# Kernel tuning notes

Hardware: AMD Instinct MI355X
Metric: run time of the kernel (lower is better)

Reference implementation:

```python
import jax, jax.numpy as jnp
import numpy as np

EMBED_DIM = 768
NUM_HEADS = 12
HEAD_DIM = EMBED_DIM // NUM_HEADS
MEMORY_SIZE = 64
B, T = 8, 1024


def setup_inputs() -> dict:
    key = jax.random.key(0)
    ks = jax.random.split(key, 8)
    s = 0.02
    return {
        "x": jax.random.normal(ks[0], (B, T, EMBED_DIM), dtype=jnp.float32),
        "w_qkv": jax.random.normal(ks[1], (EMBED_DIM, 3 * EMBED_DIM), dtype=jnp.float32) * s,
        "b_qkv": jax.random.normal(ks[2], (3 * EMBED_DIM,), dtype=jnp.float32) * s,
        "w_out": jax.random.normal(ks[3], (EMBED_DIM, EMBED_DIM), dtype=jnp.float32) * s,
        "b_out": jax.random.normal(ks[4], (EMBED_DIM,), dtype=jnp.float32) * s,
        "w_mem": jax.random.normal(ks[5], (EMBED_DIM, EMBED_DIM), dtype=jnp.float32) * s,
        "b_mem": jax.random.normal(ks[6], (EMBED_DIM,), dtype=jnp.float32) * s,
        "memory": jax.random.normal(ks[7], (1, MEMORY_SIZE, EMBED_DIM), dtype=jnp.float32),
    }


def reference(x, w_qkv, b_qkv, w_out, b_out, w_mem, b_mem, memory):
    Bx, Tx, C = x.shape
    H, D = NUM_HEADS, HEAD_DIM
    scale = 1.0 / np.sqrt(D).astype(np.float32)

    # qkv projection -> (3, B, H, T, D)
    qkv = (x @ w_qkv + b_qkv).reshape(Bx, Tx, 3, H, D)
    qkv = jnp.transpose(qkv, (2, 0, 3, 1, 4))
    q, k, v = qkv[0], qkv[1], qkv[2]

    # full (non-causal) local attention over T
    scores = jnp.einsum("bhqd,bhkd->bhqk", q, k) * scale  # (B,H,T,T)
    local_out = jnp.einsum("bhqk,bhkd->bhqd", jax.nn.softmax(scores, axis=-1), v)

    # memory attention: projected memory serves as both K and V
    mem = memory @ w_mem + b_mem                      # (1, M, C)
    mem = jnp.broadcast_to(mem, (Bx, MEMORY_SIZE, C))
    mem_kv = jnp.transpose(mem.reshape(Bx, MEMORY_SIZE, H, D), (0, 2, 1, 3))  # (B,H,M,D)
    mem_scores = jnp.einsum("bhqd,bhmd->bhqm", q, mem_kv) * scale
    mem_out = jnp.einsum("bhqm,bhmd->bhqd", jax.nn.softmax(mem_scores, axis=-1), mem_kv)

    out = (local_out + mem_out).transpose(0, 2, 1, 3).reshape(Bx, Tx, C)
    return out @ w_out + b_out
```

## Files before the change

### kernel.cpp

```cpp
#include <hip/hip_runtime.h>

#define EMBED 768
#define NH 12
#define HD 64
#define MEMN 64
#define BB 8
#define TT 1024
#define ROWS 8192
#define QKV_N 2304
#define QSZ 6291456

typedef short bf16x8_t __attribute__((ext_vector_type(8)));
typedef float f32x4_t __attribute__((ext_vector_type(4)));

__device__ __forceinline__ unsigned short f2b(float f){
    union { float f; unsigned int i; } v; v.f = f;
    unsigned int x = v.i;
    unsigned int r = x + 0x7fffu + ((x >> 16) & 1u);
    return (unsigned short)(r >> 16);
}
__device__ __forceinline__ unsigned short f2b_ru(float f){
    union { float f; unsigned int i; } v; v.f = f;
    return (unsigned short)((v.i + 0x8000u) >> 16);
}

__device__ __forceinline__ void gl16(const unsigned short* g, unsigned short* l){
    __builtin_amdgcn_global_load_lds(
        (const __attribute__((address_space(1))) void*)g,
        (__attribute__((address_space(3))) void*)l,
        16, 0, 0);
}

#define PREP_CVT   3072
#define PREP_TQKV  4800
#define PREP_TOUT  5376
#define PREP_TOTAL 5388

__global__ __launch_bounds__(256) void prep_kernel(
    const float* __restrict__ x,
    const float* __restrict__ w_qkv,
    const float* __restrict__ w_out,
    const float* __restrict__ memory,
    const float* __restrict__ w_mem,
    const float* __restrict__ b_mem,
    unsigned short* __restrict__ xb,
    unsigned short* __restrict__ wqkvT,
    unsigned short* __restrict__ woutT,
    unsigned short* __restrict__ mem_k,
    unsigned short* __restrict__ mem_v)
{
    __shared__ unsigned short pool[5120];
    const int bid = blockIdx.x;
    const int t = threadIdx.x;

    if (bid < PREP_CVT) {
        int i = bid * 2048 + t * 8;
        float4 f0 = *(const float4*)&x[i];
        float4 f1 = *(const float4*)&x[i + 4];
        union { bf16x8_t v; unsigned short s[8]; } u;
        u.s[0] = f2b(f0.x); u.s[1] = f2b(f0.y); u.s[2] = f2b(f0.z); u.s[3] = f2b(f0.w);
        u.s[4] = f2b(f1.x); u.s[5] = f2b(f1.y); u.s[6] = f2b(f1.z); u.s[7] = f2b(f1.w);
        *(bf16x8_t*)&xb[i] = u.v;
    } else if (bid < PREP_TOUT) {
        const float* in; unsigned short* out; int R, C, loc;
        if (bid < PREP_TQKV) { in = w_qkv; out = wqkvT; R = EMBED; C = QKV_N; loc = bid - PREP_CVT; }
        else                 { in = w_out; out = woutT; R = EMBED; C = EMBED; loc = bid - PREP_TQKV; }
        int nbc = C / 32;
        int bc = (loc % nbc) * 32, br = (loc / nbc) * 32;
        unsigned short (*tile)[33] = (unsigned short(*)[33])pool;
        int lr = t >> 5, lc = t & 31;
        for (int i = 0; i < 4; i++) {
            int r = lr + i * 8;
            tile[r][lc] = f2b(in[(size_t)(br + r) * C + bc + lc]);
        }
        __syncthreads();
        for (int i = 0; i < 4; i++) {
            int r = lr + i * 8;
            out[(size_t)(bc + r) * R + br + lc] = tile[lc][r];
        }
    } else {
        unsigned short (*As)[40] = (unsigned short(*)[40])pool;
        unsigned short (*Bs)[40] = (unsigned short(*)[40])(pool + 2560);
        int wave = t >> 6, lane = t & 63;
        int ln = lane & 15, lq = lane >> 4;
        int bn = (bid - PREP_TOUT) * 64;
        const int K = EMBED, N = EMBED;

        f32x4_t acc[4];
        for (int i = 0; i < 4; i++) acc[i] = (f32x4_t)(0.f);
        int sm = t >> 2, sk = (t & 3) * 8;
        int bk = t >> 3, bn8 = (t & 7) * 8;

        for (int k0 = 0; k0 < K; k0 += 32) {
            __syncthreads();
            {
                float4 f0 = *(const float4*)&memory[(size_t)sm * K + k0 + sk];
                float4 f1 = *(const float4*)&memory[(size_t)sm * K + k0 + sk + 4];
                unsigned short* ap = &As[sm][sk];
                ap[0] = f2b(f0.x); ap[1] = f2b(f0.y); ap[2] = f2b(f0.z); ap[3] = f2b(f0.w);
                ap[4] = f2b(f1.x); ap[5] = f2b(f1.y); ap[6] = f2b(f1.z); ap[7] = f2b(f1.w);
            }
            {
                float4 g0 = *(const float4*)&w_mem[(size_t)(k0 + bk) * N + bn + bn8];
                float4 g1 = *(const float4*)&w_mem[(size_t)(k0 + bk) * N + bn + bn8 + 4];
                Bs[bn8 + 0][bk] = f2b(g0.x); Bs[bn8 + 1][bk] = f2b(g0.y);
                Bs[bn8 + 2][bk] = f2b(g0.z); Bs[bn8 + 3][bk] = f2b(g0.w);
                Bs[bn8 + 4][bk] = f2b(g1.x); Bs[bn8 + 5][bk] = f2b(g1.y);
                Bs[bn8 + 6][bk] = f2b(g1.z); Bs[bn8 + 7][bk] = f2b(g1.w);
            }
            __syncthreads();
            bf16x8_t a = *(bf16x8_t*)&As[wave * 16 + ln][lq * 8];
            for (int nt = 0; nt < 4; nt++) {
                bf16x8_t bf = *(bf16x8_t*)&Bs[nt * 16 + ln][lq * 8];
                acc[nt] = __builtin_amdgcn_mfma_f32_16x16x32_bf16(a, bf, acc[nt], 0, 0, 0);
            }
        }
        for (int nt = 0; nt < 4; nt++) {
            int c = bn + nt * 16 + ln;
            float bv = b_mem[c];
            for (int r = 0; r < 4; r++) {
                int row = wave * 16 + lq * 4 + r;
                int h = c >> 6, d = c & 63;
                unsigned short o = f2b(acc[nt][r] + bv);
                mem_k[((h * 64 + row) << 6) + d] = o;
                mem_v[((h * 64 + d) << 6) + row] = o;
            }
        }
    }
}

__global__ __launch_bounds__(256) void vtrans_kernel(
    const unsigned short* __restrict__ in, unsigned short* __restrict__ out)
{
    __shared__ unsigned short tile[64][72];
    int t0 = blockIdx.x * 64;
    int bh = blockIdx.y;
    const unsigned short* ip = in + ((size_t)bh * TT + t0) * 64;
    unsigned short* op = out + ((size_t)bh * 64) * TT + t0;
    int t = threadIdx.x;
    for (int i = 0; i < 2; i++) {
        int idx = i * 256 + t;
        int r = idx >> 3, c8 = (idx & 7) * 8;
        *(bf16x8_t*)&tile[r][c8] = *(const bf16x8_t*)&ip[(size_t)r * 64 + c8];
    }
    __syncthreads();
    for (int i = 0; i < 2; i++) {
        int idx = i * 256 + t;
        int d = idx >> 3, tc8 = (idx & 7) * 8;
        union { bf16x8_t v; unsigned short s[8]; } u;
        for (int j = 0; j < 8; j++) u.s[j] = tile[tc8 + j][d];
        *(bf16x8_t*)&op[(size_t)d * TT + tc8] = u.v;
    }
}

__global__ __launch_bounds__(512) void gemm512(
    const unsigned short* __restrict__ A,
    const unsigned short* __restrict__ BT,
    const float* __restrict__ bias,
    unsigned short* __restrict__ dq,
    unsigned short* __restrict__ dkv,
    int M, int N, int K)
{
    __shared__ unsigned short As[2][16384];
    __shared__ unsigned short Bs[2][8192];
    const int t = threadIdx.x;
    const int wave = t >> 6, lane = t & 63;
    const int ln = lane & 15, lq = lane >> 4;
    const int wm = (wave >> 1) * 64, wn = (wave & 1) * 64;

    int bid0 = blockIdx.y * gridDim.x + blockIdx.x;
    int bid = (bid0 & 7) * 72 + (bid0 >> 3);
    int by = bid / 18, bx = bid - by * 18;
    const int bm = by * 256, bn = bx * 128;

    f32x4_t acc[4][4];
    for (int i = 0; i < 4; i++)
        for (int j = 0; j < 4; j++) acc[i][j] = (f32x4_t)(0.f);

    const int rl8 = lane >> 3;
    const int swz = ((lane & 7) ^ rl8) * 8;
    const unsigned short* Ap = A + (size_t)(bm + wave * 32 + rl8) * K + swz;
    const unsigned short* Bp = BT + (size_t)(bn + wave * 16 + rl8) * K + swz;

    const int e0 = (lq ^ (ln & 7)) * 8;
    const int e1 = e0 ^ 32;

    auto compute = [&](const unsigned short* Ac, const unsigned short* Bc) {
        bf16x8_t af0[4], af1[4], bf0[4], bf1[4];
#pragma unroll
        for (int mt = 0; mt < 4; mt++) {
            af0[mt] = *(const bf16x8_t*)&Ac[(wm + mt * 16 + ln) * 64 + e0];
            af1[mt] = *(const bf16x8_t*)&Ac[(wm + mt * 16 + ln) * 64 + e1];
        }
#pragma unroll
        for (int nt = 0; nt < 4; nt++) {
            bf0[nt] = *(const bf16x8_t*)&Bc[(wn + nt * 16 + ln) * 64 + e0];
            bf1[nt] = *(const bf16x8_t*)&Bc[(wn + nt * 16 + ln) * 64 + e1];
        }
        __builtin_amdgcn_s_setprio(1);
#pragma unroll
        for (int mt = 0; mt < 4; mt++)
#pragma unroll
            for (int nt = 0; nt < 4; nt++)
                acc[mt][nt] = __builtin_amdgcn_mfma_f32_16x16x32_bf16(
                    af0[mt], bf0[nt], acc[mt][nt], 0, 0, 0);
#pragma unroll
        for (int mt = 0; mt < 4; mt++)
#pragma unroll
            for (int nt = 0; nt < 4; nt++)
                acc[mt][nt] = __builtin_amdgcn_mfma_f32_16x16x32_bf16(
                    af1[mt], bf1[nt], acc[mt][nt], 0, 0, 0);
        __builtin_amdgcn_s_setprio(0);
    };

    for (int i = 0; i < 4; i++)
        gl16(Ap + (size_t)(i * 8) * K, &As[0][wave * 2048 + i * 512]);
    for (int i = 0; i < 2; i++)
        gl16(Bp + (size_t)(i * 8) * K, &Bs[0][wave * 1024 + i * 512]);
    __syncthreads();

    int cur = 0;
    for (int k0 = 0; k0 < K - 64; k0 += 64) {
        const int nb = cur ^ 1;
        for (int i = 0; i < 4; i++)
            gl16(Ap + (size_t)(i * 8) * K + k0 + 64, &As[nb][wave * 2048 + i * 512]);
        for (int i = 0; i < 2; i++)
            gl16(Bp + (size_t)(i * 8) * K + k0 + 64, &Bs[nb][wave * 1024 + i * 512]);
        compute(As[cur], Bs[cur]);
        __syncthreads();
        cur = nb;
    }
    compute(As[cur], Bs[cur]);

    const float QSCALE = 0.125f * 1.44269504088896340736f;
    const int s = bn / 768;
    for (int nt = 0; nt < 4; nt++) {
        int c = bn + wn + nt * 16 + ln;
        int rem = c - s * 768;
        int h = rem >> 6, d = rem & 63;
        float bv = bias[c];
        for (int mt = 0; mt < 4; mt++) {
            for (int r = 0; r < 4; r++) {
                int row = bm + wm + mt * 16 + lq * 4 + r;
                float val = acc[mt][nt][r] + bv;
                if (s == 0) {
                    dq[(size_t)row * 768 + rem] = f2b(val * QSCALE);
                } else {
                    int bb = row >> 10, tt = row & 1023;
                    dkv[(size_t)(s - 1) * QSZ +
                        (((size_t)(bb * 12 + h) * 1024 + tt) << 6) + d] = f2b(val);
                }
            }
        }
    }
}

__global__ __launch_bounds__(256) void gemm_bt(
    const unsigned short* __restrict__ A,
    const unsigned short* __restrict__ BT,
    const float* __restrict__ bias,
    float* __restrict__ df,
    int M, int N, int K)
{
    __shared__ unsigned short As[2][8192];
    __shared__ unsigned short Bs[2][8192];
    const int t = threadIdx.x;
    const int wave = t >> 6, lane = t & 63;
    const int ln = lane & 15, lq = lane >> 4;
    const int wm = (wave >> 1) * 64, wn = (wave & 1) * 64;
    const int bm = blockIdx.y * 128, bn = blockIdx.x * 128;

    f32x4_t acc[4][4];
    for (int i = 0; i < 4; i++)
        for (int j = 0; j < 4; j++) acc[i][j] = (f32x4_t)(0.f);

    const int rl8 = lane >> 3;
    const int swz = ((lane & 7) ^ rl8) * 8;
    const unsigned short* Ap = A + (size_t)(bm + wave * 32 + rl8) * K + swz;
    const unsigned short* Bp = BT + (size_t)(bn + wave * 32 + rl8) * K + swz;

    const int e0 = (lq ^ (ln & 7)) * 8;
    const int e1 = e0 ^ 32;

    auto compute = [&](const unsigned short* Ac, const unsigned short* Bc) {
        bf16x8_t af0[4], af1[4], bf0[4], bf1[4];
#pragma unroll
        for (int mt = 0; mt < 4; mt++) {
            af0[mt] = *(const bf16x8_t*)&Ac[(wm + mt * 16 + ln) * 64 + e0];
            af1[mt] = *(const bf16x8_t*)&Ac[(wm + mt * 16 + ln) * 64 + e1];
        }
#pragma unroll
        for (int nt = 0; nt < 4; nt++) {
            bf0[nt] = *(const bf16x8_t*)&Bc[(wn + nt * 16 + ln) * 64 + e0];
            bf1[nt] = *(const bf16x8_t*)&Bc[(wn + nt * 16 + ln) * 64 + e1];
        }
        __builtin_amdgcn_s_setprio(1);
#pragma unroll
        for (int mt = 0; mt < 4; mt++)
#pragma unroll
            for (int nt = 0; nt < 4; nt++)
                acc[mt][nt] = __builtin_amdgcn_mfma_f32_16x16x32_bf16(
                    af0[mt], bf0[nt], acc[mt][nt], 0, 0, 0);
#pragma unroll
        for (int mt = 0; mt < 4; mt++)
#pragma unroll
            for (int nt = 0; nt < 4; nt++)
                acc[mt][nt] = __builtin_amdgcn_mfma_f32_16x16x32_bf16(
                    af1[mt], bf1[nt], acc[mt][nt], 0, 0, 0);
        __builtin_amdgcn_s_setprio(0);
    };

    for (int i = 0; i < 4; i++) {
        gl16(Ap + (size_t)(i * 8) * K, &As[0][wave * 2048 + i * 512]);
        gl16(Bp + (size_t)(i * 8) * K, &Bs[0][wave * 2048 + i * 512]);
    }
    __syncthreads();

    int cur = 0;
    for (int k0 = 0; k0 < K - 64; k0 += 64) {
        const int nb = cur ^ 1;
        for (int i = 0; i < 4; i++) {
            gl16(Ap + (size_t)(i * 8) * K + k0 + 64, &As[nb][wave * 2048 + i * 512]);
            gl16(Bp + (size_t)(i * 8) * K + k0 + 64, &Bs[nb][wave * 2048 + i * 512]);
        }
        compute(As[cur], Bs[cur]);
        __syncthreads();
        cur = nb;
    }
    compute(As[cur], Bs[cur]);

    for (int nt = 0; nt < 4; nt++) {
        int c = bn + wn + nt * 16 + ln;
        float bv = bias[c];
        for (int mt = 0; mt < 4; mt++)
            for (int r = 0; r < 4; r++) {
                int row = bm + wm + mt * 16 + lq * 4 + r;
                df[(size_t)row * N + c] = acc[mt][nt][r] + bv;
            }
    }
}

__global__ __launch_bounds__(512) void attn_kernel(
    unsigned short* __restrict__ qio,
    const unsigned short* __restrict__ k_ws,
    const unsigned short* __restrict__ vT_ws,
    const unsigned short* __restrict__ mem_k,
    const unsigned short* __restrict__ mem_v)
{
    __shared__ unsigned short Qs[8192];
    __shared__ unsigned short Ks[8192];
    __shared__ unsigned short Vs[8192];
    unsigned short* Ps = Qs;

    const int t = threadIdx.x;
    const int wave = t >> 6, lane = t & 63;
    const int ln = lane & 15, lq = lane >> 4;
    const int rl = lane >> 3;
    const int cl = ((lane & 7) ^ rl) * 8;

    int bid = blockIdx.x;
    int xcd = bid & 7, rest = bid >> 3;
    int bh = xcd * 12 + (rest >> 3);
    int qt = rest & 7;
    int b = bh / 12, h = bh - b * 12;

    unsigned short* qp = qio + ((size_t)(b * TT + qt * 128)) * 768 + h * 64;
    const unsigned short* kp = k_ws + (size_t)bh * TT * 64;
    const unsigned short* vp = vT_ws + ((size_t)bh << 16);
    const unsigned short* mkp = mem_k + h * 4096;
    const unsigned short* mvp = mem_v + h * 4096;

    {
        const unsigned short* qg = qp + (size_t)(wave * 16 + rl) * 768 + cl;
        gl16(qg, &Qs[wave * 1024]);
        gl16(qg + (size_t)8 * 768, &Qs[wave * 1024 + 512]);
    }
    __syncthreads();
    const int e0 = (lq ^ (ln & 7)) * 8;
    const int e1 = ((lq ^ (ln & 7)) ^ 4) * 8;
    bf16x8_t aq0 = *(bf16x8_t*)&Qs[(wave * 16 + ln) * 64 + e0];
    bf16x8_t aq1 = *(bf16x8_t*)&Qs[(wave * 16 + ln) * 64 + e1];

    const unsigned short* kg = kp + (wave * 16 + rl) * 64 + cl;
    const unsigned short* vg = vp + (size_t)((wave & 3) * 16 + rl) * 1024 + (wave >> 2) * 64 + cl;

    const int hi3 = ln >> 3, lo3 = ln & 7;
    const int pm = (lq & 1) << 2;
    const int pw0 = (wave * 16 + lq * 4) * 64 + lo3;

    float lsum[4] = {0.f, 0.f, 0.f, 0.f};
    f32x4_t accO[4];
    for (int nt = 0; nt < 4; nt++) accO[nt] = (f32x4_t)(0.f);

    for (int kt = 0; kt < 8; kt++) {
        __syncthreads();
        gl16(kg + kt * 8192,        &Ks[wave * 1024]);
        gl16(kg + kt * 8192 + 512,  &Ks[wave * 1024 + 512]);
        gl16(vg + kt * 128,                 &Vs[wave * 1024]);
        gl16(vg + (size_t)8 * 1024 + kt * 128, &Vs[wave * 1024 + 512]);
        __syncthreads();

        for (int half = 0; half < 2; half++) {
            const unsigned short* Kh = &Ks[half * 4096];
            const unsigned short* Vh = &Vs[half * 4096];
            f32x4_t s[4];
            for (int nt = 0; nt < 4; nt++) s[nt] = (f32x4_t)(0.f);
            for (int nt = 0; nt < 4; nt++)
                s[nt] = __builtin_amdgcn_mfma_f32_16x16x32_bf16(
                    aq0, *(bf16x8_t*)&Kh[(nt * 16 + ln) * 64 + e0], s[nt], 0, 0, 0);
            for (int nt = 0; nt < 4; nt++)
                s[nt] = __builtin_amdgcn_mfma_f32_16x16x32_bf16(
                    aq1, *(bf16x8_t*)&Kh[(nt * 16 + ln) * 64 + e1], s[nt], 0, 0, 0);

            for (int nt = 0; nt < 4; nt++) {
                for (int r = 0; r < 4; r++) {
                    float p = __builtin_amdgcn_exp2f(s[nt][r]);
                    lsum[r] += p;
                    int chp = (nt * 2 + hi3) ^ pm ^ r;
                    Ps[pw0 + r * 64 + chp * 8] = f2b_ru(p);
                }
            }
            bf16x8_t a0 = *(bf16x8_t*)&Ps[(wave * 16 + ln) * 64 + e0];
            bf16x8_t a1 = *(bf16x8_t*)&Ps[(wave * 16 + ln) * 64 + e1];
            for (int nt = 0; nt < 4; nt++) {
                accO[nt] = __builtin_amdgcn_mfma_f32_16x16x32_bf16(
                    a0, *(bf16x8_t*)&Vh[(nt * 16 + ln) * 64 + e0], accO[nt], 0, 0, 0);
                accO[nt] = __builtin_amdgcn_mfma_f32_16x16x32_bf16(
                    a1, *(bf16x8_t*)&Vh[(nt * 16 + ln) * 64 + e1], accO[nt], 0, 0, 0);
            }
        }
    }

    __syncthreads();
    gl16(mkp + (wave * 8 + rl) * 64 + cl, &Ks[wave * 512]);
    gl16(mvp + (wave * 8 + rl) * 64 + cl, &Vs[wave * 512]);
    __syncthreads();

    f32x4_t s2[4];
    for (int nt = 0; nt < 4; nt++) s2[nt] = (f32x4_t)(0.f);
    for (int nt = 0; nt < 4; nt++)
        s2[nt] = __builtin_amdgcn_mfma_f32_16x16x32_bf16(
            aq0, *(bf16x8_t*)&Ks[(nt * 16 + ln) * 64 + e0], s2[nt], 0, 0, 0);
    for (int nt = 0; nt < 4; nt++)
        s2[nt] = __builtin_amdgcn_mfma_f32_16x16x32_bf16(
            aq1, *(bf16x8_t*)&Ks[(nt * 16 + ln) * 64 + e1], s2[nt], 0, 0, 0);

    float l2[4] = {0.f, 0.f, 0.f, 0.f};
    for (int nt = 0; nt < 4; nt++) {
        for (int r = 0; r < 4; r++) {
            float p = __builtin_amdgcn_exp2f(s2[nt][r]);
            l2[r] += p;
            int chp = (nt * 2 + hi3) ^ pm ^ r;
            Ps[pw0 + r * 64 + chp * 8] = f2b_ru(p);
        }
    }
    f32x4_t accM[4];
    for (int nt = 0; nt < 4; nt++) accM[nt] = (f32x4_t)(0.f);
    {
        bf16x8_t a0 = *(bf16x8_t*)&Ps[(wave * 16 + ln) * 64 + e0];
        bf16x8_t a1 = *(bf16x8_t*)&Ps[(wave * 16 + ln) * 64 + e1];
        for (int nt = 0; nt < 4; nt++) {
            accM[nt] = __builtin_amdgcn_mfma_f32_16x16x32_bf16(
                a0, *(bf16x8_t*)&Vs[(nt * 16 + ln) * 64 + e0], accM[nt], 0, 0, 0);
            accM[nt] = __builtin_amdgcn_mfma_f32_16x16x32_bf16(
                a1, *(bf16x8_t*)&Vs[(nt * 16 + ln) * 64 + e1], accM[nt], 0, 0, 0);
        }
    }

    float inv[4], inv2[4];
    for (int r = 0; r < 4; r++) {
        float a = lsum[r], c = l2[r];
        a += __shfl_xor(a, 1); a += __shfl_xor(a, 2);
        a += __shfl_xor(a, 4); a += __shfl_xor(a, 8);
        c += __shfl_xor(c, 1); c += __shfl_xor(c, 2);
        c += __shfl_xor(c, 4); c += __shfl_xor(c, 8);
        inv[r] = 1.f / a;
        inv2[r] = 1.f / c;
    }

    for (int nt = 0; nt < 4; nt++) {
        for (int r = 0; r < 4; r++) {
            int lrow = wave * 16 + lq * 4 + r;
            int lcol = nt * 16 + ln;
            float val = accO[nt][r] * inv[r] + accM[nt][r] * inv2[r];
            qp[(size_t)lrow * 768 + lcol] = f2b(val);
        }
    }
}

extern "C" void kernel_launch(void* const* d_in, const int* in_sizes, int n_in,
                              void* d_out, int out_size, void* d_ws, size_t ws_size,
                              hipStream_t stream) {
    const float* x      = (const float*)d_in[0];
    const float* w_qkv  = (const float*)d_in[1];
    const float* b_qkv  = (const float*)d_in[2];
    const float* w_out  = (const float*)d_in[3];
    const float* b_out  = (const float*)d_in[4];
    const float* w_mem  = (const float*)d_in[5];
    const float* b_mem  = (const float*)d_in[6];
    const float* memory = (const float*)d_in[7];

    unsigned short* ws = (unsigned short*)d_ws;
    unsigned short* q_ws   = ws;
    unsigned short* k_ws   = ws + (size_t)QSZ;
    unsigned short* woutT  = ws + 3 * (size_t)QSZ;
    unsigned short* mem_k  = woutT + (size_t)EMBED * EMBED;
    unsigned short* mem_v  = mem_k + (size_t)NH * MEMN * HD;

    unsigned short* xb    = (unsigned short*)d_out;
    unsigned short* wqkvT = xb + (size_t)QSZ;
    unsigned short* vT    = (unsigned short*)d_out;

    prep_kernel<<<PREP_TOTAL, 256, 0, stream>>>(
        x, w_qkv, w_out, memory, w_mem, b_mem, xb, wqkvT, woutT, mem_k, mem_v);

    gemm512<<<dim3(QKV_N / 128, ROWS / 256), 512, 0, stream>>>(
        xb, wqkvT, b_qkv, q_ws, k_ws, ROWS, QKV_N, EMBED);

    vtrans_kernel<<<dim3(TT / 64, BB * NH), 256, 0, stream>>>(k_ws + (size_t)QSZ, vT);

    attn_kernel<<<8 * NH * BB, 512, 0, stream>>>(q_ws, k_ws, vT, mem_k, mem_v);

    gemm_bt<<<dim3(EMBED / 128, ROWS / 128), 256, 0, stream>>>(
        q_ws, woutT, b_out, (float*)d_out, ROWS, EMBED, EMBED);
}
```

Baseline: 251.1 us.

## Pipeline GEMM K-loop two stages deep with explicit vmcnt waits and fixed K

Both GEMM kernels now issue the global-to-LDS loads for two K tiles before computing, and use explicit s_waitcnt vmcnt counts with raw s_barrier and sched_barrier fences in place of __syncthreads. This keeps one tile's loads in flight while the other is computed. K is hardcoded to 768 with a fixed trip count, which removes loop overhead and lets the loop unroll. The intent is to hide global load latency and avoid the full waitcnt that __syncthreads implies, at the cost of hardcoding K=768 and depending on the exact vmcnt bookkeeping being correct.

```diff
diff --git a/kernel.cpp b/kernel.cpp
--- a/kernel.cpp
+++ b/kernel.cpp
@@ -30,6 +30,8 @@
         (__attribute__((address_space(3))) void*)l,
         16, 0, 0);
 }
+
+#define SCHED_FENCE() __builtin_amdgcn_sched_barrier(0)
 
 #define PREP_CVT   3072
 #define PREP_TQKV  4800
@@ -179,11 +181,20 @@
 
     const int rl8 = lane >> 3;
     const int swz = ((lane & 7) ^ rl8) * 8;
-    const unsigned short* Ap = A + (size_t)(bm + wave * 32 + rl8) * K + swz;
-    const unsigned short* Bp = BT + (size_t)(bn + wave * 16 + rl8) * K + swz;
+    const unsigned short* Ap = A + (size_t)(bm + wave * 32 + rl8) * 768 + swz;
+    const unsigned short* Bp = BT + (size_t)(bn + wave * 16 + rl8) * 768 + swz;
 
     const int e0 = (lq ^ (ln & 7)) * 8;
     const int e1 = e0 ^ 32;
+
+    auto stage = [&](int buf, int k0) {
+#pragma unroll
+        for (int i = 0; i < 4; i++)
+            gl16(Ap + (size_t)(i * 8) * 768 + k0, &As[buf][wave * 2048 + i * 512]);
+#pragma unroll
+        for (int i = 0; i < 2; i++)
+            gl16(Bp + (size_t)(i * 8) * 768 + k0, &Bs[buf][wave * 1024 + i * 512]);
+    };
 
     auto compute = [&](const unsigned short* Ac, const unsigned short* Bc) {
         bf16x8_t af0[4], af1[4], bf0[4], bf1[4];
@@ -213,24 +224,35 @@
         __builtin_amdgcn_s_setprio(0);
     };
 
-    for (int i = 0; i < 4; i++)
-        gl16(Ap + (size_t)(i * 8) * K, &As[0][wave * 2048 + i * 512]);
-    for (int i = 0; i < 2; i++)
-        gl16(Bp + (size_t)(i * 8) * K, &Bs[0][wave * 1024 + i * 512]);
-    __syncthreads();
-
-    int cur = 0;
-    for (int k0 = 0; k0 < K - 64; k0 += 64) {
-        const int nb = cur ^ 1;
-        for (int i = 0; i < 4; i++)
-            gl16(Ap + (size_t)(i * 8) * K + k0 + 64, &As[nb][wave * 2048 + i * 512]);
-        for (int i = 0; i < 2; i++)
-            gl16(Bp + (size_t)(i * 8) * K + k0 + 64, &Bs[nb][wave * 1024 + i * 512]);
-        compute(As[cur], Bs[cur]);
-        __syncthreads();
-        cur = nb;
-    }
-    compute(As[cur], Bs[cur]);
+    stage(0, 0);
+    stage(1, 64);
+    SCHED_FENCE();
+    asm volatile("s_waitcnt vmcnt(6)" ::: "memory");
+    SCHED_FENCE();
+    __builtin_amdgcn_s_barrier();
+    SCHED_FENCE();
+
+#pragma unroll 2
+    for (int tt = 0; tt < 10; ++tt) {
+        const int cur = tt & 1;
+        compute(&As[cur][0], &Bs[cur][0]);
+        SCHED_FENCE();
+        __builtin_amdgcn_s_barrier();
+        SCHED_FENCE();
+        stage(cur, (tt + 2) * 64);
+        SCHED_FENCE();
+        asm volatile("s_waitcnt vmcnt(6)" ::: "memory");
+        SCHED_FENCE();
+        __builtin_amdgcn_s_barrier();
+        SCHED_FENCE();
+    }
+    compute(&As[0][0], &Bs[0][0]);
+    SCHED_FENCE();
+    asm volatile("s_waitcnt vmcnt(0)" ::: "memory");
+    SCHED_FENCE();
+    __builtin_amdgcn_s_barrier();
+    SCHED_FENCE();
+    compute(&As[1][0], &Bs[1][0]);
 
     const float QSCALE = 0.125f * 1.44269504088896340736f;
     const int s = bn / 768;
@@ -246,9 +268,9 @@
                 if (s == 0) {
                     dq[(size_t)row * 768 + rem] = f2b(val * QSCALE);
                 } else {
-                    int bb = row >> 10, tt = row & 1023;
+                    int bb = row >> 10, tt2 = row & 1023;
                     dkv[(size_t)(s - 1) * QSZ +
-                        (((size_t)(bb * 12 + h) * 1024 + tt) << 6) + d] = f2b(val);
+                        (((size_t)(bb * 12 + h) * 1024 + tt2) << 6) + d] = f2b(val);
                 }
             }
         }
@@ -276,11 +298,19 @@
 
     const int rl8 = lane >> 3;
     const int swz = ((lane & 7) ^ rl8) * 8;
-    const unsigned short* Ap = A + (size_t)(bm + wave * 32 + rl8) * K + swz;
-    const unsigned short* Bp = BT + (size_t)(bn + wave * 32 + rl8) * K + swz;
+    const unsigned short* Ap = A + (size_t)(bm + wave * 32 + rl8) * 768 + swz;
+    const unsigned short* Bp = BT + (size_t)(bn + wave * 32 + rl8) * 768 + swz;
 
     const int e0 = (lq ^ (ln & 7)) * 8;
     const int e1 = e0 ^ 32;
+
+    auto stage = [&](int buf, int k0) {
+#pragma unroll
+        for (int i = 0; i < 4; i++) {
+            gl16(Ap + (size_t)(i * 8) * 768 + k0, &As[buf][wave * 2048 + i * 512]);
+            gl16(Bp + (size_t)(i * 8) * 768 + k0, &Bs[buf][wave * 2048 + i * 512]);
+        }
+    };
 
     auto compute = [&](const unsigned short* Ac, const unsigned short* Bc) {
         bf16x8_t af0[4], af1[4], bf0[4], bf1[4];
@@ -310,24 +340,35 @@
         __builtin_amdgcn_s_setprio(0);
     };
 
-    for (int i = 0; i < 4; i++) {
-        gl16(Ap + (size_t)(i * 8) * K, &As[0][wave * 2048 + i * 512]);
-        gl16(Bp + (size_t)(i * 8) * K, &Bs[0][wave * 2048 + i * 512]);
-    }
-    __syncthreads();
-
-    int cur = 0;
-    for (int k0 = 0; k0 < K - 64; k0 += 64) {
-        const int nb = cur ^ 1;
-        for (int i = 0; i < 4; i++) {
-            gl16(Ap + (size_t)(i * 8) * K + k0 + 64, &As[nb][wave * 2048 + i * 512]);
-            gl16(Bp + (size_t)(i * 8) * K + k0 + 64, &Bs[nb][wave * 2048 + i * 512]);
-        }
-        compute(As[cur], Bs[cur]);
-        __syncthreads();
-        cur = nb;
-    }
-    compute(As[cur], Bs[cur]);
+    stage(0, 0);
+    stage(1, 64);
+    SCHED_FENCE();
+    asm volatile("s_waitcnt vmcnt(8)" ::: "memory");
+    SCHED_FENCE();
+    __builtin_amdgcn_s_barrier();
+    SCHED_FENCE();
+
+#pragma unroll 2
+    for (int tt = 0; tt < 10; ++tt) {
+        const int cur = tt & 1;
+        compute(&As[cur][0], &Bs[cur][0]);
+        SCHED_FENCE();
+        __builtin_amdgcn_s_barrier();
+        SCHED_FENCE();
+        stage(cur, (tt + 2) * 64);
+        SCHED_FENCE();
+        asm volatile("s_waitcnt vmcnt(8)" ::: "memory");
+        SCHED_FENCE();
+        __builtin_amdgcn_s_barrier();
+        SCHED_FENCE();
+    }
+    compute(&As[0][0], &Bs[0][0]);
+    SCHED_FENCE();
+    asm volatile("s_waitcnt vmcnt(0)" ::: "memory");
+    SCHED_FENCE();
+    __builtin_amdgcn_s_barrier();
+    SCHED_FENCE();
+    compute(&As[1][0], &Bs[1][0]);
 
     for (int nt = 0; nt < 4; nt++) {
         int c = bn + wn + nt * 16 + ln;
```

Measured after the change: 246.5 us. About the same (-1.9%).
